# Kernel tuning notes

Measured on AMD Instinct MI355X. Metric: run time of the kernel, lower is better.

## Reference

```python
import jax, jax.numpy as jnp
import numpy as np

NUM_OPS = 8
D = 1024
B = 8192


def setup_inputs() -> dict:
    key = jax.random.key(0)
    k1, k2, k3, k4 = jax.random.split(key, 4)
    x = jax.random.normal(k1, (B, D), dtype=jnp.float32)
    logits = 0.001 * jax.random.normal(k2, (NUM_OPS,), dtype=jnp.float32)
    Ws = jax.random.normal(k3, (NUM_OPS, D, D), dtype=jnp.float32) * (1.0 / np.sqrt(D))
    bs = jax.random.normal(k4, (NUM_OPS, D), dtype=jnp.float32) * 0.01
    return {"x": x, "logits": logits, "Ws": Ws, "bs": bs, "num_on_samples": 2}


def reference(x, logits, Ws, bs, num_on_samples):
    # non_stochastic_call: top-k op selection by architecture logits,
    # dispatch x to the selected ops, sum-combine the results.
    _, top_k_ids = jax.lax.top_k(logits, num_on_samples)  # [k]
    W_sel = jnp.take(Ws, top_k_ids, axis=0)  # [k, D, D]
    b_sel = jnp.take(bs, top_k_ids, axis=0)  # [k, D]
    # each op is Dense(D->D) + relu: [k, B, D]
    op_results = jax.nn.relu(jnp.einsum('bd,kde->kbe', x, W_sel) + b_sel[:, None, :])
    return jnp.sum(op_results, axis=0)  # [B, D]
```

## Files before the change

kernel.cpp:

```cpp
#include <hip/hip_runtime.h>
#include <hip/hip_bf16.h>

#define NUM_OPS 8
#define D 1024
#define B_ROWS 8192

typedef unsigned short ushort_t;
typedef __attribute__((ext_vector_type(8))) short bf16x8;
typedef __attribute__((ext_vector_type(4))) float f32x4;
typedef __attribute__((ext_vector_type(4))) float float4v;
typedef __attribute__((ext_vector_type(8))) unsigned short ushort8;

__device__ __forceinline__ unsigned short f2bf(float f) {
    union { float f; unsigned int u; } v; v.f = f;
    unsigned int u = v.u;
    unsigned int lsb = (u >> 16) & 1u;
    u += 0x7fffu + lsb;
    return (unsigned short)(u >> 16);
}

__device__ __forceinline__ void load_lds16(const void* g, void* l) {
    __builtin_amdgcn_global_load_lds(
        (const __attribute__((address_space(1))) void*)g,
        (__attribute__((address_space(3))) void*)l,
        16, 0, 0);
}

__global__ void topk_kernel(const float* __restrict__ logits, int* __restrict__ idx) {
    if (threadIdx.x == 0 && blockIdx.x == 0) {
        float best = -__builtin_inff(); int bi = 0;
        for (int i = 0; i < NUM_OPS; ++i) {
            float v = logits[i];
            if (v > best) { best = v; bi = i; }
        }
        float best2 = -__builtin_inff(); int bi2 = 0;
        for (int i = 0; i < NUM_OPS; ++i) {
            if (i == bi) continue;
            float v = logits[i];
            if (v > best2) { best2 = v; bi2 = i; }
        }
        idx[0] = bi; idx[1] = bi2;
    }
}

__global__ void convert_x(const float* __restrict__ x, ushort_t* __restrict__ xb) {
    int i = (blockIdx.x * 256 + threadIdx.x) * 8;
    float4v v0 = *(const float4v*)(x + i);
    float4v v1 = *(const float4v*)(x + i + 4);
    ushort8 o;
    o[0] = f2bf(v0[0]); o[1] = f2bf(v0[1]); o[2] = f2bf(v0[2]); o[3] = f2bf(v0[3]);
    o[4] = f2bf(v1[0]); o[5] = f2bf(v1[1]); o[6] = f2bf(v1[2]); o[7] = f2bf(v1[3]);
    *(ushort8*)(xb + i) = o;
}

__global__ void gather_transpose_W(const float* __restrict__ Ws,
                                   const int* __restrict__ idx,
                                   ushort_t* __restrict__ Wt) {
    __shared__ float t[32][33];
    int e    = blockIdx.x >> 10;
    int tile = blockIdx.x & 1023;
    int td = (tile >> 5) << 5;
    int te = (tile & 31) << 5;
    int tx = threadIdx.x & 31, ty = threadIdx.x >> 5;
    const float* W = Ws + (size_t)idx[e] * D * D;
    for (int r = 0; r < 4; ++r)
        t[ty + 8 * r][tx] = W[(size_t)(td + ty + 8 * r) * D + te + tx];
    __syncthreads();
    ushort_t* o = Wt + (size_t)e * D * D;
    for (int r = 0; r < 4; ++r)
        o[(size_t)(te + ty + 8 * r) * D + td + tx] = f2bf(t[tx][ty + 8 * r]);
}

__device__ __forceinline__ void stage_half_A(const ushort_t* __restrict__ Abf,
                                             int brow, int t, ushort_t* dstbuf,
                                             int h, int tid, int wv) {
    #pragma unroll
    for (int i = 0; i < 2; ++i) {
        const int c   = i * 512 + tid;
        const int rr  = c >> 3;
        const int cb  = (c & 7) * 16;
        const int gcb = cb ^ ((rr & 7) << 4);
        const ushort_t* g = Abf + (size_t)(brow + h * 128 + rr) * D + t * 64 + (gcb >> 1);
        ushort_t* l = dstbuf + (h * 16384 + (i * 512 + wv * 64) * 16) / 2;
        load_lds16(g, l);
    }
}

__device__ __forceinline__ void stage_half_B(const ushort_t* __restrict__ Wt,
                                             int bcolIdx, int t, ushort_t* dstbuf,
                                             int h, int tid, int wv) {
    #pragma unroll
    for (int i = 0; i < 2; ++i) {
        const int c   = i * 512 + tid;
        const int rr  = c >> 3;
        const int cb  = (c & 7) * 16;
        const int gcb = cb ^ ((rr & 7) << 4);
        const ushort_t* g = Wt + (size_t)h * D * D
                          + (size_t)(bcolIdx * 128 + rr) * D + t * 64 + (gcb >> 1);
        ushort_t* l = dstbuf + (h * 16384 + (i * 512 + wv * 64) * 16) / 2;
        load_lds16(g, l);
    }
}

#define BAR()   do { __builtin_amdgcn_s_barrier(); __builtin_amdgcn_sched_barrier(0); } while (0)
#define LGKM0() do { asm volatile("s_waitcnt lgkmcnt(0)" ::: "memory"); __builtin_amdgcn_sched_barrier(0); } while (0)
#define VM(N)   do { asm volatile("s_waitcnt vmcnt(" #N ")" ::: "memory"); __builtin_amdgcn_sched_barrier(0); } while (0)
#define PRIO1() __builtin_amdgcn_s_setprio(1)
#define PRIO0() __builtin_amdgcn_s_setprio(0)

#define DS_A(mh)                                                                   \
    do {                                                                           \
        _Pragma("unroll") for (int kk = 0; kk < 2; ++kk)                           \
        _Pragma("unroll") for (int m = 0; m < 4; ++m)                              \
            af[kk][m] = *(const bf16x8*)(curA +                                    \
                (size_t)(((mh) * 128 + wr * 64 + m * 16 + l15) * 128) +            \
                (kk ? x1 : x0));                                                   \
    } while (0)

#define DS_B(E)                                                                    \
    do {                                                                           \
        _Pragma("unroll") for (int kk = 0; kk < 2; ++kk)                           \
        _Pragma("unroll") for (int n = 0; n < 2; ++n)                              \
            bfr[E][kk][n] = *(const bf16x8*)(curB +                                \
                (size_t)(((E) * 128 + wc * 32 + n * 16 + l15) * 128) +             \
                (kk ? x1 : x0));                                                   \
    } while (0)

#define MM(E, mh)                                                                  \
    do {                                                                           \
        _Pragma("unroll") for (int kk = 0; kk < 2; ++kk)                           \
        _Pragma("unroll") for (int m = 0; m < 4; ++m)                              \
        _Pragma("unroll") for (int n = 0; n < 2; ++n)                              \
            acc[E][(mh) * 4 + m][n] = __builtin_amdgcn_mfma_f32_16x16x32_bf16(     \
                af[kk][m], bfr[E][kk][n], acc[E][(mh) * 4 + m][n], 0, 0, 0);       \
    } while (0)

__global__ __launch_bounds__(512, 2)
void gemm_dual(const ushort_t* __restrict__ Abf, const ushort_t* __restrict__ Wt,
               const float* __restrict__ bs, const int* __restrict__ idx,
               float* __restrict__ out) {
    constexpr int NT = D / 64;
    __shared__ __align__(16) ushort_t ldsA[2][256 * 64];
    __shared__ __align__(16) ushort_t ldsB[2][256 * 64];

    const int tid  = threadIdx.x;
    const int wv   = tid >> 6;
    const int lane = tid & 63;
    const int wr   = wv >> 2, wc = wv & 3;
    const int l15  = lane & 15, lq = lane >> 4;
    const int swz  = (lane & 7) << 4;
    const int x0   = (lq * 16) ^ swz;
    const int x1   = (64 + lq * 16) ^ swz;

    const int bid     = blockIdx.x;
    const int brow    = (bid >> 3) * 256;
    const int bcolIdx = bid & 7;

    f32x4  acc[2][8][2] = {};
    bf16x8 af[2][4];
    bf16x8 bfr[2][2][2];

    stage_half_A(Abf, brow, 0, ldsA[0], 0, tid, wv);
    stage_half_B(Wt, bcolIdx, 0, ldsB[0], 0, tid, wv);
    stage_half_B(Wt, bcolIdx, 0, ldsB[0], 1, tid, wv);
    stage_half_A(Abf, brow, 0, ldsA[0], 1, tid, wv);
    stage_half_A(Abf, brow, 1, ldsA[1], 0, tid, wv);
    stage_half_B(Wt, bcolIdx, 1, ldsB[1], 1, tid, wv);
    VM(8);
    BAR();

    for (int u = 0; u < NT - 1; ++u) {
        const char* curA = (const char*)ldsA[u & 1];
        const char* curB = (const char*)ldsB[u & 1];

        DS_A(0); DS_B(0);
        if (u + 1 < NT) stage_half_B(Wt, bcolIdx, u + 1, ldsB[(u + 1) & 1], 0, tid, wv);
        BAR(); LGKM0();
        PRIO1(); MM(0, 0); PRIO0();
        VM(6); BAR();

        DS_B(1);
        if (u + 1 < NT) stage_half_A(Abf, brow, u + 1, ldsA[(u + 1) & 1], 1, tid, wv);
        BAR(); LGKM0();
        PRIO1(); MM(1, 0); PRIO0();
        VM(6); BAR();

        DS_A(1);
        if (u + 2 < NT) stage_half_A(Abf, brow, u + 2, ldsA[u & 1], 0, tid, wv);
        BAR(); LGKM0();
        PRIO1(); MM(1, 1); PRIO0();
        VM(6); BAR();

        if (u + 2 < NT) stage_half_B(Wt, bcolIdx, u + 2, ldsB[u & 1], 1, tid, wv);
        BAR(); LGKM0();
        PRIO1(); MM(0, 1); PRIO0();
        VM(6); BAR();
    }

    {
        const char* curA = (const char*)ldsA[(NT - 1) & 1];
        const char* curB = (const char*)ldsB[(NT - 1) & 1];
        VM(0); BAR();

        DS_A(0); DS_B(0);
        BAR(); LGKM0();
        PRIO1(); MM(0, 0); PRIO0();
        BAR();

        DS_B(1);
        BAR(); LGKM0();
        PRIO1(); MM(1, 0); PRIO0();
        BAR();

        DS_A(1);
        BAR(); LGKM0();
        PRIO1(); MM(1, 1); PRIO0();
        BAR();

        LGKM0();
        PRIO1(); MM(0, 1); PRIO0();
    }

    const int i0 = idx[0], i1 = idx[1];
    #pragma unroll
    for (int n = 0; n < 2; ++n) {
        const int col = bcolIdx * 128 + wc * 32 + n * 16 + l15;
        const float b0 = bs[i0 * D + col];
        const float b1 = bs[i1 * D + col];
        #pragma unroll
        for (int mh = 0; mh < 2; ++mh)
        #pragma unroll
        for (int m = 0; m < 4; ++m) {
            const int rbase = brow + mh * 128 + wr * 64 + m * 16 + lq * 4;
            #pragma unroll
            for (int i = 0; i < 4; ++i) {
                float v0 = acc[0][mh * 4 + m][n][i] + b0; v0 = v0 > 0.f ? v0 : 0.f;
                float v1 = acc[1][mh * 4 + m][n][i] + b1; v1 = v1 > 0.f ? v1 : 0.f;
                out[(size_t)(rbase + i) * D + col] = v0 + v1;
            }
        }
    }
}

extern "C" void kernel_launch(void* const* d_in, const int* in_sizes, int n_in,
                              void* d_out, int out_size, void* d_ws, size_t ws_size,
                              hipStream_t stream) {
    const float* x      = (const float*)d_in[0];
    const float* logits = (const float*)d_in[1];
    const float* Ws     = (const float*)d_in[2];
    const float* bs     = (const float*)d_in[3];
    float* out = (float*)d_out;

    char* ws = (char*)d_ws;
    ushort_t* xbf = (ushort_t*)ws;
    ushort_t* Wt  = (ushort_t*)(ws + (size_t)B_ROWS * D * 2);
    int* idx      = (int*)(ws + (size_t)B_ROWS * D * 2 + (size_t)2 * D * D * 2);

    topk_kernel<<<1, 1, 0, stream>>>(logits, idx);
    convert_x<<<(B_ROWS * D) / (256 * 8), 256, 0, stream>>>(x, xbf);
    gather_transpose_W<<<2 * (D / 32) * (D / 32), 256, 0, stream>>>(Ws, idx, Wt);

    gemm_dual<<<256, 512, 0, stream>>>(xbf, Wt, bs, idx, out);
}
```

Before: 58.27 us.

## Restructure GEMM main loop to one barrier per k-step and remap block order

The main loop now synchronises once per k-tile. The whole next A/B tile is prefetched into the alternate LDS buffer, and partial lgkmcnt waits let MFMA work start while the remaining LDS fragment reads are still outstanding. This replaces the previous four-barrier-per-step schedule, which staggered half-tile loads two steps ahead. Block indices are also remapped so that consecutive blocks walk down rows within one weight column block, which changes L2 locality. The trade-off is a shallower prefetch distance, so global latency may be less well hidden.

```diff
diff --git a/kernel.cpp b/kernel.cpp
--- a/kernel.cpp
+++ b/kernel.cpp
@@ -102,13 +102,14 @@
     }
 }
 
-#define BAR()   do { __builtin_amdgcn_s_barrier(); __builtin_amdgcn_sched_barrier(0); } while (0)
-#define LGKM0() do { asm volatile("s_waitcnt lgkmcnt(0)" ::: "memory"); __builtin_amdgcn_sched_barrier(0); } while (0)
-#define VM(N)   do { asm volatile("s_waitcnt vmcnt(" #N ")" ::: "memory"); __builtin_amdgcn_sched_barrier(0); } while (0)
-#define PRIO1() __builtin_amdgcn_s_setprio(1)
-#define PRIO0() __builtin_amdgcn_s_setprio(0)
-
-#define DS_A(mh)                                                                   \
+#define SB()     __builtin_amdgcn_sched_barrier(0)
+#define BAR()    do { __builtin_amdgcn_s_barrier(); SB(); } while (0)
+#define LGKM(N)  do { asm volatile("s_waitcnt lgkmcnt(" #N ")" ::: "memory"); SB(); } while (0)
+#define VM(N)    do { asm volatile("s_waitcnt vmcnt(" #N ")" ::: "memory"); } while (0)
+#define PRIO1()  __builtin_amdgcn_s_setprio(1)
+#define PRIO0()  __builtin_amdgcn_s_setprio(0)
+
+#define RD_A(mh)                                                                   \
     do {                                                                           \
         _Pragma("unroll") for (int kk = 0; kk < 2; ++kk)                           \
         _Pragma("unroll") for (int m = 0; m < 4; ++m)                              \
@@ -117,7 +118,7 @@
                 (kk ? x1 : x0));                                                   \
     } while (0)
 
-#define DS_B(E)                                                                    \
+#define RD_B(E)                                                                    \
     do {                                                                           \
         _Pragma("unroll") for (int kk = 0; kk < 2; ++kk)                           \
         _Pragma("unroll") for (int n = 0; n < 2; ++n)                              \
@@ -153,8 +154,8 @@
     const int x1   = (64 + lq * 16) ^ swz;
 
     const int bid     = blockIdx.x;
-    const int brow    = (bid >> 3) * 256;
-    const int bcolIdx = bid & 7;
+    const int brow    = (bid & 31) * 256;
+    const int bcolIdx = bid >> 5;
 
     f32x4  acc[2][8][2] = {};
     bf16x8 af[2][4];
@@ -162,63 +163,54 @@
 
     stage_half_A(Abf, brow, 0, ldsA[0], 0, tid, wv);
     stage_half_B(Wt, bcolIdx, 0, ldsB[0], 0, tid, wv);
+    stage_half_A(Abf, brow, 0, ldsA[0], 1, tid, wv);
     stage_half_B(Wt, bcolIdx, 0, ldsB[0], 1, tid, wv);
-    stage_half_A(Abf, brow, 0, ldsA[0], 1, tid, wv);
-    stage_half_A(Abf, brow, 1, ldsA[1], 0, tid, wv);
-    stage_half_B(Wt, bcolIdx, 1, ldsB[1], 1, tid, wv);
-    VM(8);
-    BAR();
+    VM(0);
 
     for (int u = 0; u < NT - 1; ++u) {
         const char* curA = (const char*)ldsA[u & 1];
         const char* curB = (const char*)ldsB[u & 1];
-
-        DS_A(0); DS_B(0);
-        if (u + 1 < NT) stage_half_B(Wt, bcolIdx, u + 1, ldsB[(u + 1) & 1], 0, tid, wv);
-        BAR(); LGKM0();
+        ushort_t* nA = ldsA[(u & 1) ^ 1];
+        ushort_t* nB = ldsB[(u & 1) ^ 1];
+
+        BAR();
+
+        RD_A(0); RD_B(0); RD_B(1);
+        stage_half_A(Abf, brow, u + 1, nA, 0, tid, wv);
+        stage_half_B(Wt, bcolIdx, u + 1, nB, 0, tid, wv);
+
+        LGKM(4);
         PRIO1(); MM(0, 0); PRIO0();
-        VM(6); BAR();
-
-        DS_B(1);
-        if (u + 1 < NT) stage_half_A(Abf, brow, u + 1, ldsA[(u + 1) & 1], 1, tid, wv);
-        BAR(); LGKM0();
+
+        stage_half_A(Abf, brow, u + 1, nA, 1, tid, wv);
+
+        LGKM(0);
         PRIO1(); MM(1, 0); PRIO0();
-        VM(6); BAR();
-
-        DS_A(1);
-        if (u + 2 < NT) stage_half_A(Abf, brow, u + 2, ldsA[u & 1], 0, tid, wv);
-        BAR(); LGKM0();
+
+        RD_A(1);
+        stage_half_B(Wt, bcolIdx, u + 1, nB, 1, tid, wv);
+
+        LGKM(0);
+        PRIO1(); MM(0, 1); PRIO0();
         PRIO1(); MM(1, 1); PRIO0();
-        VM(6); BAR();
-
-        if (u + 2 < NT) stage_half_B(Wt, bcolIdx, u + 2, ldsB[u & 1], 1, tid, wv);
-        BAR(); LGKM0();
-        PRIO1(); MM(0, 1); PRIO0();
-        VM(6); BAR();
+
+        VM(0);
     }
 
     {
         const char* curA = (const char*)ldsA[(NT - 1) & 1];
         const char* curB = (const char*)ldsB[(NT - 1) & 1];
-        VM(0); BAR();
-
-        DS_A(0); DS_B(0);
-        BAR(); LGKM0();
+
+        BAR();
+        RD_A(0); RD_B(0); RD_B(1);
+        LGKM(4);
         PRIO1(); MM(0, 0); PRIO0();
-        BAR();
-
-        DS_B(1);
-        BAR(); LGKM0();
+        LGKM(0);
         PRIO1(); MM(1, 0); PRIO0();
-        BAR();
-
-        DS_A(1);
-        BAR(); LGKM0();
+        RD_A(1);
+        LGKM(0);
+        PRIO1(); MM(0, 1); PRIO0();
         PRIO1(); MM(1, 1); PRIO0();
-        BAR();
-
-        LGKM0();
-        PRIO1(); MM(0, 1); PRIO0();
     }
 
     const int i0 = idx[0], i1 = idx[1];
```

New measurement: 55.48 us. 1.05x faster.
